# Optimization experiments

Measured on AMD Instinct MI355X. Metric: run time of the kernel, lower is better.

Reference implementation:

```python
import jax, jax.numpy as jnp
import numpy as np
from jax import lax

B, NM, P, F, E, H, K = 32, 131072, 256, 3, 64, 4, 3
DH = E // H


def layer_norm(x, gamma, beta, eps=1e-5):
    mu = x.mean(-1, keepdims=True)
    var = ((x - mu) ** 2).mean(-1, keepdims=True)
    return (x - mu) * lax.rsqrt(var + eps) * gamma + beta


def knn_interp(x, pos_x, pos_y, k=K):
    """x: [B, Nx, F] features at pos_x [Nx, 2]; interpolate to pos_y [Ny, 2].
    Positions are shared across the batch (they are tiled in the torch code),
    so KNN indices/weights are computed once. Matches torch knn + inverse-
    squared-distance weighted scatter (uniform per-batch counts => gather form).
    """
    d2 = jnp.sum((pos_y[:, None, :] - pos_x[None, :, :]) ** 2, axis=-1)  # [Ny, Nx]
    neg_d2, idx = lax.top_k(-d2, k)                                      # [Ny, k]
    w = 1.0 / jnp.clip(-neg_d2, 1e-16)                                   # [Ny, k]
    w = lax.stop_gradient(w)  # torch computes weights under no_grad
    gathered = x[:, idx, :]                                              # [B, Ny, k, F]
    num = jnp.sum(gathered * w[None, :, :, None], axis=2)                # [B, Ny, F]
    den = jnp.sum(w, axis=1)[None, :, None]                              # [1, Ny, 1]
    return num / den


def setup_inputs() -> dict:
    key = jax.random.key(0)
    ks = jax.random.split(key, 8)
    return {
        "node_attr": jax.random.normal(ks[0], (B * NM, F), jnp.float32),
        "position_mesh": jax.random.uniform(ks[1], (NM, 2), jnp.float32),
        "position_pivotal": jax.random.uniform(ks[2], (P, 2), jnp.float32),
        "ln_gamma": jnp.ones((F,), jnp.float32),
        "ln_beta": jnp.zeros((F,), jnp.float32),
        "Wf": jax.random.normal(ks[3], (E, F), jnp.float32) * (2.0 / E) ** 0.5,
        "bf": jnp.zeros((E,), jnp.float32),
        "Wp": jax.random.normal(ks[4], (E, 2), jnp.float32) * (2.0 / E) ** 0.5,
        "bp": jnp.zeros((E,), jnp.float32),
        "in_proj_w": jax.random.normal(ks[5], (3 * E, E), jnp.float32) * (1.0 / E) ** 0.5,
        "in_proj_b": jnp.zeros((3 * E,), jnp.float32),
        "batch_size": B,
    }


def reference(node_attr, position_mesh, position_pivotal, ln_gamma, ln_beta,
              Wf, bf, Wp, bp, in_proj_w, in_proj_b, batch_size):
    x = node_attr.reshape(batch_size, -1, F)                 # [B, NM, F]
    # PivotalNorm after encoder (encoder/decoder MeshGraphNet omitted: undefined dep)
    x = layer_norm(x, ln_gamma, ln_beta)
    # ---- downsample: mesh -> pivotal via inverse-distance KNN interpolation ----
    y = knn_interp(x, position_mesh, position_pivotal)       # [B, P, F]
    # attention-based pooling over pivotal nodes
    q = (jnp.einsum('bpf,ef->bpe', y, Wf) + bf
         + (position_pivotal @ Wp.T + bp)[None])             # [B, P, E]
    Wq, Wk = in_proj_w[:E], in_proj_w[E:2 * E]
    bq, bk = in_proj_b[:E], in_proj_b[E:2 * E]
    Q = (q @ Wq.T + bq).reshape(batch_size, P, H, DH)
    Kt = (q @ Wk.T + bk).reshape(batch_size, P, H, DH)
    scores = jnp.einsum('bqhd,bkhd->bhqk', Q, Kt) / np.float32(np.sqrt(DH))
    attn = jax.nn.softmax(scores, axis=-1)                   # [B, H, P, P]
    attn_w = attn.mean(axis=1)                               # avg heads, [B, P, P]
    y = jnp.einsum('bqk,bkf->bqf', attn_w, y)                # [B, P, F]
    # ---- interpolate: pivotal -> mesh ----
    out = knn_interp(y, position_pivotal, position_mesh)     # [B, NM, F]
    return out.reshape(-1, F)
```

## Files before the change

### kernel.cpp

```cpp
#include <hip/hip_runtime.h>
#include <math.h>

#define NM 131072
#define PP 256
#define BB 32
#define INF_F 3.0e38f

#define GM   64
#define GM2  (GM * GM)
#define CAPM 96
#define GP   16
#define GP2  (GP * GP)
#define CAPP 8

typedef unsigned long long u64;

__device__ __forceinline__ u64 packkey(float d, int i) {
  return ((u64)__float_as_uint(d) << 32) | (unsigned)i;
}

__device__ __forceinline__ void ins3k(u64 k, u64& k0, u64& k1, u64& k2) {
  bool l0 = k < k0, l1 = k < k1, l2 = k < k2;
  k2 = l1 ? k1 : (l2 ? k : k2);
  k1 = l0 ? k0 : (l1 ? k : k1);
  k0 = l0 ? k : k0;
}

__device__ __forceinline__ float dist2(float ax, float ay, float bx, float by) {
  float dx = ax - bx, dy = ay - by;
  return __fadd_rn(__fmul_rn(dx, dx), __fmul_rn(dy, dy));
}

__global__ __launch_bounds__(256)
void build_buckets(const float* __restrict__ mesh, const float* __restrict__ piv,
                   unsigned* __restrict__ cntM, unsigned* __restrict__ cntP,
                   unsigned* __restrict__ ovfc,
                   float* __restrict__ bufM,
                   int* __restrict__ bufP,
                   float* __restrict__ ovfM, int* __restrict__ ovfP,
                   float* __restrict__ y2) {
  const int g = blockIdx.x * 256 + threadIdx.x;
  if (g < NM) {
    float2 mp = ((const float2*)mesh)[g];
    int cx = min((int)(mp.x * GM), GM - 1);
    int cy = min((int)(mp.y * GM), GM - 1);
    int c = cy * GM + cx;
    unsigned s = atomicAdd(&cntM[c], 1u);
    if (s < CAPM) {
      float* d = bufM + (size_t)(c * CAPM + s) * 3;
      d[0] = mp.x; d[1] = mp.y; ((int*)d)[2] = g;
    } else {
      unsigned o = atomicAdd(&ovfc[0], 1u);
      float* d = ovfM + (size_t)o * 3;
      d[0] = mp.x; d[1] = mp.y; ((int*)d)[2] = g;
    }
  }
  if (blockIdx.x == 0 && threadIdx.x < PP) {
    const int p = threadIdx.x;
    float2 pv = ((const float2*)piv)[p];
    int cx = min((int)(pv.x * GP), GP - 1);
    int cy = min((int)(pv.y * GP), GP - 1);
    int c = cy * GP + cx;
    unsigned s = atomicAdd(&cntP[c], 1u);
    if (s < CAPP) bufP[c * CAPP + s] = p;
    else { unsigned o = atomicAdd(&ovfc[1], 1u); ovfP[o] = p; }
  }
  if (blockIdx.x == 1) {
    for (int j = threadIdx.x; j < BB * PP * 4; j += 256) y2[j] = 0.f;
  }
}

__global__ __launch_bounds__(256)
void knnA_grid(const float* __restrict__ piv,
               const unsigned* __restrict__ cntM, const float* __restrict__ bufM,
               const unsigned* __restrict__ ovfc, const float* __restrict__ ovfM,
               float* __restrict__ wA, int* __restrict__ idxA) {
  const int p = blockIdx.x;
  const int t = threadIdx.x;
  __shared__ u64 sk[256 * 3];
  __shared__ u64 g3[3];
  __shared__ int sdone;

  const float2 pv = ((const float2*)piv)[p];
  const int cx = min((int)(pv.x * GM), GM - 1);
  const int cy = min((int)(pv.y * GM), GM - 1);

  u64 b0 = ~0ull, b1 = ~0ull, b2 = ~0ull;

  {
    int x0 = max(cx - 1, 0), x1 = min(cx + 1, GM - 1);
    int y0 = max(cy - 1, 0), y1 = min(cy + 1, GM - 1);
    for (int yy = y0; yy <= y1; ++yy) {
      int cb = yy * GM + x0;
      int tot = (x1 - x0 + 1) * CAPM;
      for (int s = t; s < tot; s += 256) {
        int ci = s / CAPM, j = s - ci * CAPM;
        int c = cb + ci;
        if (j < (int)min(cntM[c], (unsigned)CAPM)) {
          const float* cp = bufM + (size_t)(c * CAPM + j) * 3;
          float d = dist2(pv.x, pv.y, cp[0], cp[1]);
          ins3k(packkey(d, ((const int*)cp)[2]), b0, b1, b2);
        }
      }
    }
    int no = (int)ovfc[0];
    for (int j = t; j < no; j += 256) {
      const float* cp = ovfM + (size_t)j * 3;
      float d = dist2(pv.x, pv.y, cp[0], cp[1]);
      ins3k(packkey(d, ((const int*)cp)[2]), b0, b1, b2);
    }
  }

  int R = 1;
  u64 p0 = ~0ull, p1 = ~0ull, p2 = ~0ull;
  while (true) {
    sk[t * 3 + 0] = b0; sk[t * 3 + 1] = b1; sk[t * 3 + 2] = b2;
    __syncthreads();
    if (t < 32) {
      u64 e0 = ~0ull, e1 = ~0ull, e2 = ~0ull;
#pragma unroll
      for (int s = 0; s < 8; ++s) {
        int o = (t + 32 * s) * 3;
        ins3k(sk[o], e0, e1, e2); ins3k(sk[o + 1], e0, e1, e2); ins3k(sk[o + 2], e0, e1, e2);
      }
      sk[t * 3] = e0; sk[t * 3 + 1] = e1; sk[t * 3 + 2] = e2;
    }
    __syncthreads();
    if (t == 0) {
      u64 e0 = p0, e1 = p1, e2 = p2;
      for (int s = 0; s < 32; ++s) {
        ins3k(sk[s * 3], e0, e1, e2); ins3k(sk[s * 3 + 1], e0, e1, e2); ins3k(sk[s * 3 + 2], e0, e1, e2);
      }
      g3[0] = e0; g3[1] = e1; g3[2] = e2;
      float d2f = __uint_as_float((unsigned)(e2 >> 32));
      float md = (float)R * (1.0f / GM);
      sdone = (md * md > d2f) ? 1 : 0;
    }
    __syncthreads();
    if (sdone) break;
    p0 = g3[0]; p1 = g3[1]; p2 = g3[2];
    b0 = b1 = b2 = ~0ull;
    R += 1;
    int x0 = max(cx - R, 0), x1 = min(cx + R, GM - 1);
    for (int pass = 0; pass < 2; ++pass) {
      int yy = pass ? cy + R : cy - R;
      if (yy < 0 || yy > GM - 1) continue;
      int cb = yy * GM + x0;
      int tot = (x1 - x0 + 1) * CAPM;
      for (int s = t; s < tot; s += 256) {
        int ci = s / CAPM, j = s - ci * CAPM;
        int c = cb + ci;
        if (j < (int)min(cntM[c], (unsigned)CAPM)) {
          const float* cp = bufM + (size_t)(c * CAPM + j) * 3;
          float d = dist2(pv.x, pv.y, cp[0], cp[1]);
          ins3k(packkey(d, ((const int*)cp)[2]), b0, b1, b2);
        }
      }
    }
    int yy0 = max(cy - R + 1, 0), yy1 = min(cy + R - 1, GM - 1);
    for (int pass = 0; pass < 2; ++pass) {
      int xx = pass ? cx + R : cx - R;
      if (xx < 0 || xx > GM - 1) continue;
      int tot = (yy1 - yy0 + 1) * CAPM;
      for (int s = t; s < tot; s += 256) {
        int ri = s / CAPM, j = s - ri * CAPM;
        int c = (yy0 + ri) * GM + xx;
        if (j < (int)min(cntM[c], (unsigned)CAPM)) {
          const float* cp = bufM + (size_t)(c * CAPM + j) * 3;
          float d = dist2(pv.x, pv.y, cp[0], cp[1]);
          ins3k(packkey(d, ((const int*)cp)[2]), b0, b1, b2);
        }
      }
    }
    __syncthreads();
  }
  if (t == 0) {
#pragma unroll
    for (int k = 0; k < 3; ++k) {
      u64 e = g3[k];
      float d = __uint_as_float((unsigned)(e >> 32));
      wA[p * 3 + k] = 1.0f / fmaxf(d, 1e-16f);
      idxA[p * 3 + k] = (int)(unsigned)(e & 0xffffffffu);
    }
  }
}

__global__ __launch_bounds__(128, 2)
void gather_qqk(const float* __restrict__ node, const float* __restrict__ piv,
                const float* __restrict__ gamma, const float* __restrict__ beta,
                const float* __restrict__ Wf, const float* __restrict__ bf,
                const float* __restrict__ Wp, const float* __restrict__ bp,
                const float* __restrict__ ipw, const float* __restrict__ ipb,
                const float* __restrict__ wA, const int* __restrict__ idxA,
                float* __restrict__ y, float* __restrict__ Qh, float* __restrict__ Kh) {
  const int b = blockIdx.x >> 5;
  const int ptile = (blockIdx.x & 31) * 8;
  const int t = threadIdx.x;
  __shared__ float qs[8][64];
  __shared__ float ys[8][3];

  if (t < 8) {
    const int p = ptile + t;
    const float g0 = gamma[0], g1 = gamma[1], g2 = gamma[2];
    const float be0 = beta[0], be1 = beta[1], be2 = beta[2];
    float num0 = 0.f, num1 = 0.f, num2 = 0.f, den = 0.f;
#pragma unroll
    for (int k = 0; k < 3; ++k) {
      int idx = idxA[p * 3 + k];
      float w = wA[p * 3 + k];
      const float* r = node + ((size_t)b * NM + idx) * 3;
      float a0 = r[0], a1 = r[1], a2 = r[2];
      float mu = (a0 + a1 + a2) * (1.0f / 3.0f);
      float e0 = a0 - mu, e1 = a1 - mu, e2 = a2 - mu;
      float var = (e0 * e0 + e1 * e1 + e2 * e2) * (1.0f / 3.0f);
      float sc = 1.0f / sqrtf(var + 1e-5f);
      num0 += (e0 * sc * g0 + be0) * w;
      num1 += (e1 * sc * g1 + be1) * w;
      num2 += (e2 * sc * g2 + be2) * w;
      den += w;
    }
    float o0 = num0 / den, o1 = num1 / den, o2 = num2 / den;
    ys[t][0] = o0; ys[t][1] = o1; ys[t][2] = o2;
    float* yr = y + (b * PP + p) * 3;
    yr[0] = o0; yr[1] = o1; yr[2] = o2;
  }
  __syncthreads();

  const int e = t & 63;
  const int half = t >> 6;
  {
    float wf0 = Wf[e * 3], wf1 = Wf[e * 3 + 1], wf2 = Wf[e * 3 + 2];
    float wp0 = Wp[e * 2], wp1 = Wp[e * 2 + 1];
    float cst = bf[e] + bp[e];
    for (int r = half; r < 8; r += 2) {
      int p = ptile + r;
      float pe = piv[2 * p] * wp0 + piv[2 * p + 1] * wp1;
      qs[r][e] = ys[r][0] * wf0 + ys[r][1] * wf1 + ys[r][2] * wf2 + cst + pe;
    }
  }
  __syncthreads();

  const int row = half * 64 + e;
  float wreg[64];
  const float4* W4 = (const float4*)(ipw + row * 64);
#pragma unroll
  for (int j = 0; j < 16; ++j) {
    float4 v = W4[j];
    wreg[4 * j] = v.x; wreg[4 * j + 1] = v.y; wreg[4 * j + 2] = v.z; wreg[4 * j + 3] = v.w;
  }
  float bias = ipb[row];
  float* dst = half ? Kh : Qh;
  const int h = e >> 4, d = e & 15;
  for (int r = 0; r < 8; ++r) {
    float acc = bias;
#pragma unroll
    for (int j = 0; j < 64; ++j) acc += qs[r][j] * wreg[j];
    int p = ptile + r;
    dst[(((b * 4 + h) * PP) + p) * 16 + d] = acc;
  }
}

__global__ __launch_bounds__(256, 2)
void attn_kernel(const float* __restrict__ Qh, const float* __restrict__ Kh,
                 const float* __restrict__ y, float* __restrict__ y2) {
  const int b = blockIdx.x >> 4;
  const int h = (blockIdx.x >> 2) & 3;
  const int qq = blockIdx.x & 3;
  const int t = threadIdx.x;
  const int sub = t & 7;
  const int rt = t >> 3;

  __shared__ float4 sK[PP * 5];
  __shared__ float4 sY[PP];

  {
    const float4* src = (const float4*)(Kh + (size_t)(b * 4 + h) * PP * 16);
#pragma unroll
    for (int i = t; i < PP * 4; i += 256) {
      int k = i >> 2, j = i & 3;
      sK[k * 5 + j] = src[i];
    }
    const float* yr = y + (b * PP + t) * 3;
    sY[t] = make_float4(yr[0], yr[1], yr[2], 0.f);
  }
  __syncthreads();

  const int q0 = qq * 64 + rt * 2;
  const float4* q4 = (const float4*)(Qh + ((size_t)((b * 4 + h) * PP) + q0) * 16);
  float4 A0 = q4[0], A1 = q4[1], A2 = q4[2], A3 = q4[3];
  float4 B0 = q4[4], B1 = q4[5], B2 = q4[6], B3 = q4[7];

  float m0 = -INF_F, l0 = 0.f, x0 = 0.f, x1 = 0.f, x2 = 0.f;
  float m1 = -INF_F, l1 = 0.f, z0 = 0.f, z1 = 0.f, z2 = 0.f;

#pragma unroll 4
  for (int kk = 0; kk < 32; ++kk) {
    int k = kk * 8 + sub;
    float4 K0 = sK[k * 5 + 0], K1 = sK[k * 5 + 1], K2 = sK[k * 5 + 2], K3 = sK[k * 5 + 3];
    float4 yv = sY[k];
    float s0 = (A0.x*K0.x + A0.y*K0.y + A0.z*K0.z + A0.w*K0.w
              + A1.x*K1.x + A1.y*K1.y + A1.z*K1.z + A1.w*K1.w
              + A2.x*K2.x + A2.y*K2.y + A2.z*K2.z + A2.w*K2.w
              + A3.x*K3.x + A3.y*K3.y + A3.z*K3.z + A3.w*K3.w) * 0.25f;
    float s1 = (B0.x*K0.x + B0.y*K0.y + B0.z*K0.z + B0.w*K0.w
              + B1.x*K1.x + B1.y*K1.y + B1.z*K1.z + B1.w*K1.w
              + B2.x*K2.x + B2.y*K2.y + B2.z*K2.z + B2.w*K2.w
              + B3.x*K3.x + B3.y*K3.y + B3.z*K3.z + B3.w*K3.w) * 0.25f;
    {
      float mn = fmaxf(m0, s0);
      float p = __expf(s0 - mn), sc = __expf(m0 - mn);
      l0 = l0 * sc + p;
      x0 = x0 * sc + p * yv.x; x1 = x1 * sc + p * yv.y; x2 = x2 * sc + p * yv.z;
      m0 = mn;
    }
    {
      float mn = fmaxf(m1, s1);
      float p = __expf(s1 - mn), sc = __expf(m1 - mn);
      l1 = l1 * sc + p;
      z0 = z0 * sc + p * yv.x; z1 = z1 * sc + p * yv.y; z2 = z2 * sc + p * yv.z;
      m1 = mn;
    }
  }

#pragma unroll
  for (int off = 1; off < 8; off <<= 1) {
    float mo = __shfl_xor(m0, off), lo = __shfl_xor(l0, off);
    float b0 = __shfl_xor(x0, off), b1 = __shfl_xor(x1, off), b2 = __shfl_xor(x2, off);
    float M = fmaxf(m0, mo);
    float es = __expf(m0 - M), eo = __expf(mo - M);
    l0 = l0 * es + lo * eo;
    x0 = x0 * es + b0 * eo; x1 = x1 * es + b1 * eo; x2 = x2 * es + b2 * eo;
    m0 = M;

    float mo1 = __shfl_xor(m1, off), lo1 = __shfl_xor(l1, off);
    float c0 = __shfl_xor(z0, off), c1 = __shfl_xor(z1, off), c2 = __shfl_xor(z2, off);
    float M1 = fmaxf(m1, mo1);
    float es1 = __expf(m1 - M1), eo1 = __expf(mo1 - M1);
    l1 = l1 * es1 + lo1 * eo1;
    z0 = z0 * es1 + c0 * eo1; z1 = z1 * es1 + c1 * eo1; z2 = z2 * es1 + c2 * eo1;
    m1 = M1;
  }

  if (sub == 0) {
    float inv0 = 0.25f / l0;
    float inv1 = 0.25f / l1;
    float* o0 = y2 + (size_t)(b * PP + q0) * 4;
    atomicAdd(o0 + 0, x0 * inv0);
    atomicAdd(o0 + 1, x1 * inv0);
    atomicAdd(o0 + 2, x2 * inv0);
    float* o1 = o0 + 4;
    atomicAdd(o1 + 0, z0 * inv1);
    atomicAdd(o1 + 1, z1 * inv1);
    atomicAdd(o1 + 2, z2 * inv1);
  }
}

__global__ __launch_bounds__(256)
void interp_knnB_out(const float* __restrict__ mesh, const float* __restrict__ piv,
                     const unsigned* __restrict__ cntP, const int* __restrict__ bufP,
                     const unsigned* __restrict__ ovfc, const int* __restrict__ ovfP,
                     const float* __restrict__ y2, float* __restrict__ out) {
  const int t = threadIdx.x;
  const int mt = blockIdx.x >> 2;
  const int bg = blockIdx.x & 3;
  __shared__ float spx[PP], spy[PP];
  __shared__ unsigned scnt[GP2];
  __shared__ int sbuf[GP2 * CAPP];
  {
    float2 pvv = ((const float2*)piv)[t];
    spx[t] = pvv.x; spy[t] = pvv.y;
    scnt[t] = cntP[t];
    for (int j = t; j < GP2 * CAPP; j += 256) sbuf[j] = bufP[j];
  }
  __syncthreads();

  const int m = mt * 256 + t;
  const float2 mv = ((const float2*)mesh)[m];
  const int cx = min((int)(mv.x * GP), GP - 1);
  const int cy = min((int)(mv.y * GP), GP - 1);
  u64 k0 = ~0ull, k1 = ~0ull, k2 = ~0ull;

  {
    int x0 = max(cx - 2, 0), x1 = min(cx + 2, GP - 1);
    int y0 = max(cy - 2, 0), y1 = min(cy + 2, GP - 1);
    for (int yy = y0; yy <= y1; ++yy)
      for (int xx = x0; xx <= x1; ++xx) {
        int c = yy * GP + xx;
        int n = (int)min(scnt[c], (unsigned)CAPP);
        for (int j = 0; j < n; ++j) {
          int qq = sbuf[c * CAPP + j];
          float d = dist2(mv.x, mv.y, spx[qq], spy[qq]);
          ins3k(packkey(d, qq), k0, k1, k2);
        }
      }
    int no = (int)ovfc[1];
    for (int j = 0; j < no; ++j) {
      int qq = ovfP[j];
      float d = dist2(mv.x, mv.y, spx[qq], spy[qq]);
      ins3k(packkey(d, qq), k0, k1, k2);
    }
  }
  int R = 2;
  while (true) {
    float d2f = __uint_as_float((unsigned)(k2 >> 32));
    float md = (float)R * (1.0f / GP);
    if (md * md > d2f) break;
    R += 1;
    if (R >= 2 * GP) break;
    int x0 = max(cx - R, 0), x1 = min(cx + R, GP - 1);
    for (int pass = 0; pass < 2; ++pass) {
      int yy = pass ? cy + R : cy - R;
      if (yy < 0 || yy > GP - 1) continue;
      for (int xx = x0; xx <= x1; ++xx) {
        int c = yy * GP + xx;
        int n = (int)min(scnt[c], (unsigned)CAPP);
        for (int j = 0; j < n; ++j) {
          int qq = sbuf[c * CAPP + j];
          float d = dist2(mv.x, mv.y, spx[qq], spy[qq]);
          ins3k(packkey(d, qq), k0, k1, k2);
        }
      }
    }
    int yy0 = max(cy - R + 1, 0), yy1 = min(cy + R - 1, GP - 1);
    for (int pass = 0; pass < 2; ++pass) {
      int xx = pass ? cx + R : cx - R;
      if (xx < 0 || xx > GP - 1) continue;
      for (int yy = yy0; yy <= yy1; ++yy) {
        int c = yy * GP + xx;
        int n = (int)min(scnt[c], (unsigned)CAPP);
        for (int j = 0; j < n; ++j) {
          int qq = sbuf[c * CAPP + j];
          float d = dist2(mv.x, mv.y, spx[qq], spy[qq]);
          ins3k(packkey(d, qq), k0, k1, k2);
        }
      }
    }
  }

  float d0 = __uint_as_float((unsigned)(k0 >> 32));
  float d1 = __uint_as_float((unsigned)(k1 >> 32));
  float d2v = __uint_as_float((unsigned)(k2 >> 32));
  const int j0 = (int)(unsigned)(k0 & 0xffffffffu);
  const int j1 = (int)(unsigned)(k1 & 0xffffffffu);
  const int j2 = (int)(unsigned)(k2 & 0xffffffffu);
  float w0 = 1.0f / fmaxf(d0, 1e-16f);
  float w1 = 1.0f / fmaxf(d1, 1e-16f);
  float w2 = 1.0f / fmaxf(d2v, 1e-16f);
  float inv = 1.0f / (w0 + w1 + w2);

  const float4* y4 = (const float4*)y2;
#pragma unroll
  for (int i = 0; i < 8; ++i) {
    const int b = bg * 8 + i;
    const int rb = b * PP;
    float4 r0 = y4[rb + j0];
    float4 r1 = y4[rb + j1];
    float4 r2 = y4[rb + j2];
    float3 res;
    res.x = (w0 * r0.x + w1 * r1.x + w2 * r2.x) * inv;
    res.y = (w0 * r0.y + w1 * r1.y + w2 * r2.y) * inv;
    res.z = (w0 * r0.z + w1 * r1.z + w2 * r2.z) * inv;
    *(float3*)(out + ((size_t)b * NM + m) * 3) = res;
  }
}

extern "C" void kernel_launch(void* const* d_in, const int* in_sizes, int n_in,
                              void* d_out, int out_size, void* d_ws, size_t ws_size,
                              hipStream_t stream) {
  const float* node  = (const float*)d_in[0];
  const float* mesh  = (const float*)d_in[1];
  const float* piv   = (const float*)d_in[2];
  const float* gamma = (const float*)d_in[3];
  const float* beta  = (const float*)d_in[4];
  const float* Wf    = (const float*)d_in[5];
  const float* bf    = (const float*)d_in[6];
  const float* Wp    = (const float*)d_in[7];
  const float* bp    = (const float*)d_in[8];
  const float* ipw   = (const float*)d_in[9];
  const float* ipb   = (const float*)d_in[10];
  float* out = (float*)d_out;

  unsigned* cntM = (unsigned*)d_ws;
  unsigned* cntP = cntM + 4096;
  unsigned* ovfc = cntP + 256;
  float* bufM = (float*)d_ws + 4608;
  int*   bufP = (int*)(bufM + (size_t)GM2 * CAPM * 3);
  float* ovfM = (float*)(bufP + GP2 * CAPP);
  int*   ovfP = (int*)(ovfM + (size_t)NM * 3);
  float* wA   = (float*)(ovfP + PP);
  int*   idxA = (int*)(wA + PP * 3);
  float* y    = (float*)(idxA + PP * 3);
  float* Qh   = y + BB * PP * 3;
  float* Kh   = Qh + BB * PP * 64;
  float* y2   = Kh + BB * PP * 64;

  hipMemsetAsync(cntM, 0, 4608 * sizeof(unsigned), stream);
  build_buckets<<<NM / 256, 256, 0, stream>>>(mesh, piv, cntM, cntP, ovfc,
                                              bufM, bufP, ovfM, ovfP, y2);
  knnA_grid<<<PP, 256, 0, stream>>>(piv, cntM, bufM, ovfc, ovfM, wA, idxA);
  gather_qqk<<<BB * 32, 128, 0, stream>>>(node, piv, gamma, beta, Wf, bf, Wp, bp, ipw, ipb,
                                          wA, idxA, y, Qh, Kh);
  attn_kernel<<<BB * 4 * 4, 256, 0, stream>>>(Qh, Kh, y, y2);
  interp_knnB_out<<<NM / 256 * 4, 256, 0, stream>>>(mesh, piv, cntP, bufP, ovfc, ovfP, y2, out);
}
```

Before: 209.8 us.

## Split mesh KNN search from output interpolation and stage y2 in LDS

The pivotal-to-mesh KNN search is moved into its own kernel that runs once per mesh node and stores weights and indices to workspace. Before, the search was repeated in each of the four batch-group blocks. The output kernel now loads each 8-batch slice of y2 into shared memory and gathers from LDS instead of global memory. This cuts the redundant search work, at the cost of an extra launch and an extra round trip of 32 bytes per mesh node through global memory.

```diff
diff --git a/kernel.cpp b/kernel.cpp
--- a/kernel.cpp
+++ b/kernel.cpp
@@ -356,13 +356,11 @@
 }
 
 __global__ __launch_bounds__(256)
-void interp_knnB_out(const float* __restrict__ mesh, const float* __restrict__ piv,
-                     const unsigned* __restrict__ cntP, const int* __restrict__ bufP,
-                     const unsigned* __restrict__ ovfc, const int* __restrict__ ovfP,
-                     const float* __restrict__ y2, float* __restrict__ out) {
+void knnB_search(const float* __restrict__ mesh, const float* __restrict__ piv,
+                 const unsigned* __restrict__ cntP, const int* __restrict__ bufP,
+                 const unsigned* __restrict__ ovfc, const int* __restrict__ ovfP,
+                 float4* __restrict__ wB4, int4* __restrict__ idxB4) {
   const int t = threadIdx.x;
-  const int mt = blockIdx.x >> 2;
-  const int bg = blockIdx.x & 3;
   __shared__ float spx[PP], spy[PP];
   __shared__ unsigned scnt[GP2];
   __shared__ int sbuf[GP2 * CAPP];
@@ -374,7 +372,7 @@
   }
   __syncthreads();
 
-  const int m = mt * 256 + t;
+  const int m = blockIdx.x * 256 + t;
   const float2 mv = ((const float2*)mesh)[m];
   const int cx = min((int)(mv.x * GP), GP - 1);
   const int cy = min((int)(mv.y * GP), GP - 1);
@@ -440,26 +438,45 @@
   float d0 = __uint_as_float((unsigned)(k0 >> 32));
   float d1 = __uint_as_float((unsigned)(k1 >> 32));
   float d2v = __uint_as_float((unsigned)(k2 >> 32));
-  const int j0 = (int)(unsigned)(k0 & 0xffffffffu);
-  const int j1 = (int)(unsigned)(k1 & 0xffffffffu);
-  const int j2 = (int)(unsigned)(k2 & 0xffffffffu);
   float w0 = 1.0f / fmaxf(d0, 1e-16f);
   float w1 = 1.0f / fmaxf(d1, 1e-16f);
   float w2 = 1.0f / fmaxf(d2v, 1e-16f);
   float inv = 1.0f / (w0 + w1 + w2);
-
-  const float4* y4 = (const float4*)y2;
+  wB4[m] = make_float4(w0, w1, w2, inv);
+  idxB4[m] = make_int4((int)(unsigned)(k0 & 0xffffffffu),
+                       (int)(unsigned)(k1 & 0xffffffffu),
+                       (int)(unsigned)(k2 & 0xffffffffu), 0);
+}
+
+__global__ __launch_bounds__(256)
+void interp_out(const float4* __restrict__ y2, const float4* __restrict__ wB4,
+                const int4* __restrict__ idxB4, float* __restrict__ out) {
+  const int t = threadIdx.x;
+  const int mt = blockIdx.x >> 2;
+  const int bg = blockIdx.x & 3;
+  __shared__ float4 sy[8 * PP];
+  {
+    const float4* src = y2 + bg * 8 * PP;
+#pragma unroll
+    for (int j = 0; j < 8; ++j) sy[t + 256 * j] = src[t + 256 * j];
+  }
+  __syncthreads();
+
+  const int m = mt * 256 + t;
+  const float4 w = wB4[m];
+  const int4 ix = idxB4[m];
+
 #pragma unroll
   for (int i = 0; i < 8; ++i) {
+    const float4* yb = sy + i * PP;
+    float4 r0 = yb[ix.x];
+    float4 r1 = yb[ix.y];
+    float4 r2 = yb[ix.z];
+    float3 res;
+    res.x = (w.x * r0.x + w.y * r1.x + w.z * r2.x) * w.w;
+    res.y = (w.x * r0.y + w.y * r1.y + w.z * r2.y) * w.w;
+    res.z = (w.x * r0.z + w.y * r1.z + w.z * r2.z) * w.w;
     const int b = bg * 8 + i;
-    const int rb = b * PP;
-    float4 r0 = y4[rb + j0];
-    float4 r1 = y4[rb + j1];
-    float4 r2 = y4[rb + j2];
-    float3 res;
-    res.x = (w0 * r0.x + w1 * r1.x + w2 * r2.x) * inv;
-    res.y = (w0 * r0.y + w1 * r1.y + w2 * r2.y) * inv;
-    res.z = (w0 * r0.z + w1 * r1.z + w2 * r2.z) * inv;
     *(float3*)(out + ((size_t)b * NM + m) * 3) = res;
   }
 }
@@ -493,13 +510,16 @@
   float* Qh   = y + BB * PP * 3;
   float* Kh   = Qh + BB * PP * 64;
   float* y2   = Kh + BB * PP * 64;
+  float4* wB4   = (float4*)(y2 + BB * PP * 4);
+  int4*   idxB4 = (int4*)(wB4 + NM);
 
   hipMemsetAsync(cntM, 0, 4608 * sizeof(unsigned), stream);
   build_buckets<<<NM / 256, 256, 0, stream>>>(mesh, piv, cntM, cntP, ovfc,
                                               bufM, bufP, ovfM, ovfP, y2);
   knnA_grid<<<PP, 256, 0, stream>>>(piv, cntM, bufM, ovfc, ovfM, wA, idxA);
+  knnB_search<<<NM / 256, 256, 0, stream>>>(mesh, piv, cntP, bufP, ovfc, ovfP, wB4, idxB4);
   gather_qqk<<<BB * 32, 128, 0, stream>>>(node, piv, gamma, beta, Wf, bf, Wp, bp, ipw, ipb,
                                           wA, idxA, y, Qh, Kh);
   attn_kernel<<<BB * 4 * 4, 256, 0, stream>>>(Qh, Kh, y, y2);
-  interp_knnB_out<<<NM / 256 * 4, 256, 0, stream>>>(mesh, piv, cntP, bufP, ovfc, ovfP, y2, out);
-}
+  interp_out<<<NM / 256 * 4, 256, 0, stream>>>((const float4*)y2, wB4, idxB4, out);
+}
```

After: 195.0 us. 1.08x faster.
